# Optimization experiments

Measured on AMD Instinct MI355X. Metric: run time of the kernel, lower is better.

## Reference

```python
import jax, jax.numpy as jnp
import numpy as np

N = 12000       # num nodes
E = 384000      # num edges (avg degree 32)
F_IN = 512      # num_feats
H = 64          # gnn_hid_dim (== anchor_dim)
C = 7           # num_cls
SIGMA = 1.0


def setup_inputs() -> dict:
    key = jax.random.key(0)
    ks = jax.random.split(key, 9)
    scale = lambda fan_in: 1.0 / np.sqrt(fan_in)
    return {
        "x": jax.random.normal(ks[0], (N, F_IN), dtype=jnp.float32),
        "W1": jax.random.normal(ks[1], (F_IN, H), dtype=jnp.float32) * scale(F_IN),
        "b1": jnp.zeros((H,), dtype=jnp.float32),
        "W2": jax.random.normal(ks[2], (H, H), dtype=jnp.float32) * scale(H),
        "b2": jnp.zeros((H,), dtype=jnp.float32),
        "aux": jax.random.normal(ks[3], (H,), dtype=jnp.float32),
        "clf_W": jax.random.normal(ks[4], (2 * H, C), dtype=jnp.float32) * scale(2 * H),
        "clf_b": jnp.zeros((C,), dtype=jnp.float32),
        "edge_index": jax.random.randint(ks[5], (2, E), 0, N, dtype=jnp.int64),
    }


def gcn_conv(x, W, b, src, dst, n):
    # GCNConv: D^{-1/2} (A + I) D^{-1/2} X W + b, with self-loops
    h = x @ W                                                   # [N, out]
    deg = jax.ops.segment_sum(jnp.ones(src.shape[0], h.dtype), dst,
                              num_segments=n) + 1.0             # +1 for self-loop
    inv_sqrt = jax.lax.rsqrt(deg)
    norm = inv_sqrt[src] * inv_sqrt[dst]                        # [E]
    agg = jax.ops.segment_sum(h[src] * norm[:, None], dst, num_segments=n)
    agg = agg + h / deg[:, None]                                # self-loop term (norm = 1/deg)
    return agg + b


def reference(x, W1, b1, W2, b2, aux, clf_W, clf_b, edge_index):
    src, dst = edge_index[0], edge_index[1]
    n = x.shape[0]
    h = jax.nn.relu(gcn_conv(x, W1, b1, src, dst, n))
    h = gcn_conv(h, W2, b2, src, dst, n)                        # [N, H]
    # kernel aggregate: pairwise Gaussian kernel on cosine scores
    a = aux / jnp.maximum(jnp.linalg.norm(aux), 1e-12)          # F.normalize
    hn = jnp.maximum(jnp.linalg.norm(h, axis=-1), 1e-8)         # cosine_similarity eps
    score = (h @ a) / hn                                        # [N]
    diff = score[None, :] - score[:, None]                      # [N, N]
    kappa = jnp.exp(-(diff * diff) / (SIGMA * SIGMA))           # [N, N]
    z = (kappa @ h) / jnp.sum(kappa, axis=1, keepdims=True)     # [N, H]
    return jnp.concatenate([h, z], axis=-1) @ clf_W + clf_b     # [N, C]
```

## Files before the change

### kernel.cpp

```cpp
#include <hip/hip_runtime.h>
#include <hip/hip_bf16.h>

#define N_NODES 12000
#define N_EDGES 384000
#define F_IN 512
#define H 64
#define C_CLS 7
#define KTERMS 16
#define PAD 96
#define CSTR 32
#define MOM_BLKS 768
#define MSTR 1040
#define NB 4
#define GEMM_BLKS 188
#define FILL_BLKS 324

typedef __attribute__((ext_vector_type(8))) short bf16x8;
typedef __attribute__((ext_vector_type(4))) float f32x4;

__device__ __forceinline__ float wred_f(float x) {
    #pragma unroll
    for (int o = 32; o > 0; o >>= 1) x += __shfl_xor(x, o);
    return x;
}

__global__ __launch_bounds__(256) void init_k(const float* __restrict__ W1,
                                              unsigned short* __restrict__ w1Th,
                                              unsigned short* __restrict__ w1Tl,
                                              int* __restrict__ cur,
                                              double* __restrict__ M8) {
    int i = blockIdx.x * 256 + threadIdx.x;
    if (i < 64 * 512) {
        int n = i >> 9, k = i & 511;
        float v = W1[k * 64 + n];
        unsigned xb = __float_as_uint(v);
        float hf = __uint_as_float(xb & 0xffff0000u);
        w1Th[i] = (unsigned short)(xb >> 16);
        w1Tl[i] = (unsigned short)(__float_as_uint(v - hf) >> 16);
    }
    if (i < N_NODES) cur[i * CSTR] = 0;
    if (i < 8 * MSTR) M8[i] = 0.0;
}

__global__ __launch_bounds__(256) void k1_gemm_fill(const float* __restrict__ x,
                                                    const unsigned short* __restrict__ w1Th,
                                                    const unsigned short* __restrict__ w1Tl,
                                                    const int* __restrict__ ei,
                                                    float* __restrict__ hbuf,
                                                    int* __restrict__ cur,
                                                    int* __restrict__ csrc) {
    const int b = blockIdx.x, t = threadIdx.x;
    if (b < GEMM_BLKS) {
        __shared__ unsigned short wh[64 * 72];
        __shared__ unsigned short wl[64 * 72];
        const int l = t & 63, w = t >> 6;
        const int lm = l & 15, lk = l >> 4;
        const int i0 = b * 64;
        const int arow = min(i0 + w * 16 + lm, N_NODES - 1);
        const float* xrow = x + (size_t)arow * F_IN;
        f32x4 acc[4];
        #pragma unroll
        for (int c = 0; c < 4; ++c) acc[c] = (f32x4){0.f, 0.f, 0.f, 0.f};
        for (int kc = 0; kc < 8; ++kc) {
            #pragma unroll
            for (int q = 0; q < 2; ++q) {
                int idx = t + q * 256;
                int n = idx >> 3, kg = idx & 7;
                *(uint4*)(&wh[n * 72 + kg * 8]) =
                    *(const uint4*)(w1Th + n * 512 + kc * 64 + kg * 8);
                *(uint4*)(&wl[n * 72 + kg * 8]) =
                    *(const uint4*)(w1Tl + n * 512 + kc * 64 + kg * 8);
            }
            __syncthreads();
            #pragma unroll
            for (int ks = 0; ks < 2; ++ks) {
                float4 v0 = *(const float4*)(xrow + kc * 64 + ks * 32 + lk * 8);
                float4 v1 = *(const float4*)(xrow + kc * 64 + ks * 32 + lk * 8 + 4);
                float xv[8] = {v0.x, v0.y, v0.z, v0.w, v1.x, v1.y, v1.z, v1.w};
                bf16x8 ah, al;
                #pragma unroll
                for (int j = 0; j < 8; ++j) {
                    unsigned xb = __float_as_uint(xv[j]);
                    float hf = __uint_as_float(xb & 0xffff0000u);
                    ah[j] = (short)(xb >> 16);
                    al[j] = (short)(__float_as_uint(xv[j] - hf) >> 16);
                }
                #pragma unroll
                for (int c = 0; c < 4; ++c) {
                    bf16x8 bh = *(const bf16x8*)(&wh[(c * 16 + lm) * 72 + ks * 32 + lk * 8]);
                    bf16x8 bl = *(const bf16x8*)(&wl[(c * 16 + lm) * 72 + ks * 32 + lk * 8]);
                    acc[c] = __builtin_amdgcn_mfma_f32_16x16x32_bf16(ah, bh, acc[c], 0, 0, 0);
                    acc[c] = __builtin_amdgcn_mfma_f32_16x16x32_bf16(ah, bl, acc[c], 0, 0, 0);
                    acc[c] = __builtin_amdgcn_mfma_f32_16x16x32_bf16(al, bh, acc[c], 0, 0, 0);
                }
            }
            __syncthreads();
        }
        #pragma unroll
        for (int c = 0; c < 4; ++c) {
            #pragma unroll
            for (int r = 0; r < 4; ++r) {
                int row = i0 + w * 16 + lk * 4 + r;
                if (row < N_NODES)
                    hbuf[(size_t)row * H + c * 16 + lm] = acc[c][r];
            }
        }
    } else {
        for (int e = (b - GEMM_BLKS) * 256 + t; e < N_EDGES; e += FILL_BLKS * 256) {
            int s = ei[e];
            int d = ei[N_EDGES + e];
            int pos = atomicAdd(&cur[d * CSTR], 1);
            if (pos < PAD) csrc[d * PAD + pos] = s;
        }
    }
}

__global__ __launch_bounds__(256) void agg1_k(const float* __restrict__ hbuf,
                                              const float* __restrict__ b1,
                                              const int* __restrict__ cur,
                                              const int* __restrict__ csrc,
                                              float* __restrict__ h1) {
    __shared__ int2 sPair[NB * PAD];
    __shared__ int sDeg[NB];
    __shared__ float sIsd[NB];
    const int t = threadIdx.x, f = t & 63, w = t >> 6;
    const int base = blockIdx.x * NB;
    if (t < NB) {
        int d = cur[(base + t) * CSTR];
        sDeg[t] = min(d, PAD);
        sIsd[t] = rsqrtf((float)d + 1.f);
    }
    __syncthreads();
    for (int idx = t; idx < NB * PAD; idx += 256) {
        int n = idx / PAD, e = idx - n * PAD;
        if (e < sDeg[n]) {
            int s = csrc[(base + n) * PAD + e];
            sPair[idx] = make_int2(s, __float_as_int(rsqrtf((float)cur[s * CSTR] + 1.f)));
        }
    }
    __syncthreads();
    const int i = base + w;
    const int deg = sDeg[w];
    const float isd = sIsd[w];
    const int2* pp = sPair + w * PAD;
    float acc = 0.f;
    int e = 0;
    for (; e + 8 <= deg; e += 8) {
        int2 p0 = pp[e], p1 = pp[e+1], p2 = pp[e+2], p3 = pp[e+3];
        int2 p4 = pp[e+4], p5 = pp[e+5], p6 = pp[e+6], p7 = pp[e+7];
        acc += hbuf[p0.x * H + f] * __int_as_float(p0.y)
             + hbuf[p1.x * H + f] * __int_as_float(p1.y)
             + hbuf[p2.x * H + f] * __int_as_float(p2.y)
             + hbuf[p3.x * H + f] * __int_as_float(p3.y)
             + hbuf[p4.x * H + f] * __int_as_float(p4.y)
             + hbuf[p5.x * H + f] * __int_as_float(p5.y)
             + hbuf[p6.x * H + f] * __int_as_float(p6.y)
             + hbuf[p7.x * H + f] * __int_as_float(p7.y);
    }
    for (; e + 4 <= deg; e += 4) {
        int2 p0 = pp[e], p1 = pp[e+1], p2 = pp[e+2], p3 = pp[e+3];
        acc += hbuf[p0.x * H + f] * __int_as_float(p0.y)
             + hbuf[p1.x * H + f] * __int_as_float(p1.y)
             + hbuf[p2.x * H + f] * __int_as_float(p2.y)
             + hbuf[p3.x * H + f] * __int_as_float(p3.y);
    }
    for (; e < deg; ++e) {
        int2 p = pp[e];
        acc += hbuf[p.x * H + f] * __int_as_float(p.y);
    }
    float res = (acc + hbuf[i * H + f] * isd) * isd + b1[f];
    h1[i * H + f] = fmaxf(res, 0.f);
}

__global__ __launch_bounds__(256) void agg2_k(const float* __restrict__ h1,
                                              const float* __restrict__ W2,
                                              const float* __restrict__ b2,
                                              const float* __restrict__ aux,
                                              const int* __restrict__ cur,
                                              const int* __restrict__ csrc,
                                              float* __restrict__ h2,
                                              float* __restrict__ score) {
    __shared__ float w2s[64 * 64];
    __shared__ int2 sPair[NB * PAD];
    __shared__ int sDeg[NB];
    __shared__ float sIsd[NB];
    __shared__ float anorm[64];
    __shared__ float gsh[NB * 64];
    const int t = threadIdx.x, f = t & 63, w = t >> 6;
    const int base = blockIdx.x * NB;
    #pragma unroll
    for (int q = 0; q < 4; ++q) {
        int idx = t + q * 256;
        int r = idx >> 4, c4 = idx & 15;
        *(float4*)(&w2s[r * 64 + c4 * 4]) = *(const float4*)(W2 + r * H + c4 * 4);
    }
    if (t < NB) {
        int d = cur[(base + t) * CSTR];
        sDeg[t] = min(d, PAD);
        sIsd[t] = rsqrtf((float)d + 1.f);
    }
    if (t < 64) {
        float av = aux[t];
        anorm[t] = av * rsqrtf(fmaxf(wred_f(av * av), 1e-24f));
    }
    __syncthreads();
    for (int idx = t; idx < NB * PAD; idx += 256) {
        int n = idx / PAD, e = idx - n * PAD;
        if (e < sDeg[n]) {
            int s = csrc[(base + n) * PAD + e];
            sPair[idx] = make_int2(s, __float_as_int(rsqrtf((float)cur[s * CSTR] + 1.f)));
        }
    }
    __syncthreads();
    const int i = base + w;
    const int deg = sDeg[w];
    const float isd = sIsd[w];
    const int2* pp = sPair + w * PAD;
    float acc = 0.f;
    int e = 0;
    for (; e + 8 <= deg; e += 8) {
        int2 p0 = pp[e], p1 = pp[e+1], p2 = pp[e+2], p3 = pp[e+3];
        int2 p4 = pp[e+4], p5 = pp[e+5], p6 = pp[e+6], p7 = pp[e+7];
        acc += h1[p0.x * H + f] * __int_as_float(p0.y)
             + h1[p1.x * H + f] * __int_as_float(p1.y)
             + h1[p2.x * H + f] * __int_as_float(p2.y)
             + h1[p3.x * H + f] * __int_as_float(p3.y)
             + h1[p4.x * H + f] * __int_as_float(p4.y)
             + h1[p5.x * H + f] * __int_as_float(p5.y)
             + h1[p6.x * H + f] * __int_as_float(p6.y)
             + h1[p7.x * H + f] * __int_as_float(p7.y);
    }
    for (; e + 4 <= deg; e += 4) {
        int2 p0 = pp[e], p1 = pp[e+1], p2 = pp[e+2], p3 = pp[e+3];
        acc += h1[p0.x * H + f] * __int_as_float(p0.y)
             + h1[p1.x * H + f] * __int_as_float(p1.y)
             + h1[p2.x * H + f] * __int_as_float(p2.y)
             + h1[p3.x * H + f] * __int_as_float(p3.y);
    }
    for (; e < deg; ++e) {
        int2 p = pp[e];
        acc += h1[p.x * H + f] * __int_as_float(p.y);
    }
    float g = (acc + h1[i * H + f] * isd) * isd;
    gsh[w * 64 + f] = g;
    __builtin_amdgcn_wave_barrier();
    float hv = b2[f];
    #pragma unroll 16
    for (int k = 0; k < 64; ++k) hv += gsh[w * 64 + k] * w2s[k * 64 + f];
    h2[i * H + f] = hv;
    float dp = wred_f(hv * anorm[f]);
    float nn = wred_f(hv * hv);
    if (f == 0) score[i] = dp / fmaxf(sqrtf(nn), 1e-8f);
}

__global__ __launch_bounds__(256) void momden_k(const float* __restrict__ h2,
                                                const float* __restrict__ score,
                                                double* __restrict__ M8) {
    const int t = threadIdx.x, f = t & 63, g = t >> 6;
    float accM[KTERMS], accD[KTERMS];
    #pragma unroll
    for (int k = 0; k < KTERMS; ++k) { accM[k] = 0.f; accD[k] = 0.f; }
    for (int j = blockIdx.x * 4 + g; j < N_NODES; j += MOM_BLKS * 4) {
        float sj = score[j];
        float wj = expf(-sj * sj);
        float hv = h2[j * H + f];
        float tm = wj * hv, td = wj;
        #pragma unroll
        for (int k = 0; k < KTERMS; ++k) {
            accM[k] += tm; tm *= sj;
            accD[k] += td; td *= sj;
        }
    }
    __shared__ float Msh[4 * KTERMS * 64];
    __shared__ float Dsh[4 * KTERMS];
    #pragma unroll
    for (int k = 0; k < KTERMS; ++k) Msh[(g * KTERMS + k) * 64 + f] = accM[k];
    if (f == 0) {
        #pragma unroll
        for (int k = 0; k < KTERMS; ++k) Dsh[g * KTERMS + k] = accD[k];
    }
    __syncthreads();
    double* Mc = M8 + (size_t)(blockIdx.x & 7) * MSTR;
    for (int idx = t; idx < KTERMS * 64; idx += 256) {
        int k = idx >> 6, ff = idx & 63;
        float sum = Msh[(0 * KTERMS + k) * 64 + ff] + Msh[(1 * KTERMS + k) * 64 + ff]
                  + Msh[(2 * KTERMS + k) * 64 + ff] + Msh[(3 * KTERMS + k) * 64 + ff];
        unsafeAtomicAdd(&Mc[idx], (double)sum);
    }
    if (t < KTERMS) {
        float sum = Dsh[t] + Dsh[KTERMS + t] + Dsh[2 * KTERMS + t] + Dsh[3 * KTERMS + t];
        unsafeAtomicAdd(&Mc[1024 + t], (double)sum);
    }
}

__global__ __launch_bounds__(256) void final_k(const float* __restrict__ h2,
                                               const float* __restrict__ score,
                                               const double* __restrict__ M8,
                                               const float* __restrict__ clfW,
                                               const float* __restrict__ clfb,
                                               float* __restrict__ out) {
    __shared__ float Ms[KTERMS * 64];
    __shared__ float m0s[KTERMS];
    __shared__ float cw[128 * C_CLS];
    __shared__ float cb[8];
    __shared__ float zh[4 * 128];
    const int t = threadIdx.x, f = t & 63, w = t >> 6;
    for (int idx = t; idx < KTERMS * 64; idx += 256) {
        double s = 0.0;
        #pragma unroll
        for (int c = 0; c < 8; ++c) s += M8[(size_t)c * MSTR + idx];
        Ms[idx] = (float)s;
    }
    if (t < KTERMS) {
        double s = 0.0;
        #pragma unroll
        for (int c = 0; c < 8; ++c) s += M8[(size_t)c * MSTR + 1024 + t];
        m0s[t] = (float)s;
    }
    for (int idx = t; idx < 128 * C_CLS; idx += 256) cw[idx] = clfW[idx];
    if (t < C_CLS) cb[t] = clfb[t];
    __syncthreads();
    const int base = blockIdx.x * 16;
    for (int q = 0; q < 4; ++q) {
        int i = base + q * 4 + w;
        float s = score[i];
        float c = expf(-s * s);
        float t2 = 2.f * s;
        float num = 0.f, den = 0.f;
        #pragma unroll
        for (int k = 0; k < KTERMS; ++k) {
            num += c * Ms[k * 64 + f];
            den += c * m0s[k];
            c *= t2 * (1.0f / (float)(k + 1));
        }
        zh[w * 128 + f] = h2[i * H + f];
        zh[w * 128 + 64 + f] = num / den;
        __builtin_amdgcn_wave_barrier();
        if (f < C_CLS) {
            float o = cb[f];
            #pragma unroll 8
            for (int u = 0; u < 128; ++u) o += zh[w * 128 + u] * cw[u * C_CLS + f];
            out[(size_t)i * C_CLS + f] = o;
        }
        __builtin_amdgcn_wave_barrier();
    }
}

extern "C" void kernel_launch(void* const* d_in, const int* in_sizes, int n_in,
                              void* d_out, int out_size, void* d_ws, size_t ws_size,
                              hipStream_t stream) {
    (void)in_sizes; (void)n_in; (void)out_size; (void)ws_size;
    const float* x    = (const float*)d_in[0];
    const float* W1   = (const float*)d_in[1];
    const float* b1   = (const float*)d_in[2];
    const float* W2   = (const float*)d_in[3];
    const float* b2   = (const float*)d_in[4];
    const float* aux  = (const float*)d_in[5];
    const float* clfW = (const float*)d_in[6];
    const float* clfb = (const float*)d_in[7];
    const int*   ei   = (const int*)d_in[8];
    float* out = (float*)d_out;
    char* ws = (char*)d_ws;

    float*  hbuf  = (float*)(ws + 0);
    float*  h1    = (float*)(ws + 3072000);
    float*  h2    = (float*)(ws + 6144000);
    float*  score = (float*)(ws + 9216000);
    int*    csrc  = (int*)  (ws + 9264000);
    int*    cur   = (int*)  (ws + 13872000);
    double* M8    = (double*)(ws + 15408000);
    unsigned short* w1Th = (unsigned short*)(ws + 15474560);
    unsigned short* w1Tl = (unsigned short*)(ws + 15540096);

    init_k<<<128, 256, 0, stream>>>(W1, w1Th, w1Tl, cur, M8);
    k1_gemm_fill<<<GEMM_BLKS + FILL_BLKS, 256, 0, stream>>>(x, w1Th, w1Tl, ei,
                                                            hbuf, cur, csrc);
    agg1_k<<<N_NODES / NB, 256, 0, stream>>>(hbuf, b1, cur, csrc, h1);
    agg2_k<<<N_NODES / NB, 256, 0, stream>>>(h1, W2, b2, aux, cur, csrc, h2, score);
    momden_k<<<MOM_BLKS, 256, 0, stream>>>(h2, score, M8);
    final_k<<<750, 256, 0, stream>>>(h2, score, M8, clfW, clfb, out);
}
```

Measured before the change: 93.66 us.

## Fuse moment accumulation into second aggregation kernel and widen final blocks

The separate moment/denominator kernel is removed. Each agg2 block now computes the per-node power-series terms for its 4 nodes right after the score, reduces them in shared memory (aliased over the W2 tile) and adds them with fp64 atomics into 16 stripes instead of 8. This saves one kernel launch and a second pass over h2 and score. The cost is that atomic traffic grows from 768 blocks' worth of partial sums to 3000 blocks' worth, which may contend on L2. final_k now uses 250 blocks of 48 nodes each, to amortise the larger 16-stripe reduction it repeats in every block.

New measurement: 107.2 us. +14.4%, slower.

```diff
diff --git a/kernel.cpp b/kernel.cpp
--- a/kernel.cpp
+++ b/kernel.cpp
@@ -9,7 +9,7 @@
 #define KTERMS 16
 #define PAD 96
 #define CSTR 32
-#define MOM_BLKS 768
+#define NSTRIPE 16
 #define MSTR 1040
 #define NB 4
 #define GEMM_BLKS 188
@@ -28,7 +28,7 @@
                                               unsigned short* __restrict__ w1Th,
                                               unsigned short* __restrict__ w1Tl,
                                               int* __restrict__ cur,
-                                              double* __restrict__ M8) {
+                                              double* __restrict__ M16) {
     int i = blockIdx.x * 256 + threadIdx.x;
     if (i < 64 * 512) {
         int n = i >> 9, k = i & 511;
@@ -39,7 +39,7 @@
         w1Tl[i] = (unsigned short)(__float_as_uint(v - hf) >> 16);
     }
     if (i < N_NODES) cur[i * CSTR] = 0;
-    if (i < 8 * MSTR) M8[i] = 0.0;
+    for (int j = i; j < NSTRIPE * MSTR; j += 32768) M16[j] = 0.0;
 }
 
 __global__ __launch_bounds__(256) void k1_gemm_fill(const float* __restrict__ x,
@@ -172,20 +172,24 @@
     h1[i * H + f] = fmaxf(res, 0.f);
 }
 
-__global__ __launch_bounds__(256) void agg2_k(const float* __restrict__ h1,
-                                              const float* __restrict__ W2,
-                                              const float* __restrict__ b2,
-                                              const float* __restrict__ aux,
-                                              const int* __restrict__ cur,
-                                              const int* __restrict__ csrc,
-                                              float* __restrict__ h2,
-                                              float* __restrict__ score) {
-    __shared__ float w2s[64 * 64];
-    __shared__ int2 sPair[NB * PAD];
-    __shared__ int sDeg[NB];
-    __shared__ float sIsd[NB];
-    __shared__ float anorm[64];
-    __shared__ float gsh[NB * 64];
+__global__ __launch_bounds__(256) void agg2m_k(const float* __restrict__ h1,
+                                               const float* __restrict__ W2,
+                                               const float* __restrict__ b2,
+                                               const float* __restrict__ aux,
+                                               const int* __restrict__ cur,
+                                               const int* __restrict__ csrc,
+                                               float* __restrict__ h2,
+                                               float* __restrict__ score,
+                                               double* __restrict__ M16) {
+    __shared__ __align__(16) char smem[20768];
+    float* w2s   = (float*)smem;
+    int2*  sPair = (int2*)(smem + 16384);
+    int*   sDeg  = (int*)(smem + 19456);
+    float* sIsd  = (float*)(smem + 19472);
+    float* anorm = (float*)(smem + 19488);
+    float* gsh   = (float*)(smem + 19744);
+    float* Msh   = (float*)smem;
+    float* Dsh   = (float*)(smem + 16384);
     const int t = threadIdx.x, f = t & 63, w = t >> 6;
     const int base = blockIdx.x * NB;
     #pragma unroll
@@ -250,37 +254,20 @@
     h2[i * H + f] = hv;
     float dp = wred_f(hv * anorm[f]);
     float nn = wred_f(hv * hv);
-    if (f == 0) score[i] = dp / fmaxf(sqrtf(nn), 1e-8f);
-}
-
-__global__ __launch_bounds__(256) void momden_k(const float* __restrict__ h2,
-                                                const float* __restrict__ score,
-                                                double* __restrict__ M8) {
-    const int t = threadIdx.x, f = t & 63, g = t >> 6;
-    float accM[KTERMS], accD[KTERMS];
+    float sc = dp / fmaxf(sqrtf(nn), 1e-8f);
+    if (f == 0) score[i] = sc;
+    __syncthreads();
+    float wj = expf(-sc * sc);
+    float tm = wj * hv;
     #pragma unroll
-    for (int k = 0; k < KTERMS; ++k) { accM[k] = 0.f; accD[k] = 0.f; }
-    for (int j = blockIdx.x * 4 + g; j < N_NODES; j += MOM_BLKS * 4) {
-        float sj = score[j];
-        float wj = expf(-sj * sj);
-        float hv = h2[j * H + f];
-        float tm = wj * hv, td = wj;
-        #pragma unroll
-        for (int k = 0; k < KTERMS; ++k) {
-            accM[k] += tm; tm *= sj;
-            accD[k] += td; td *= sj;
-        }
-    }
-    __shared__ float Msh[4 * KTERMS * 64];
-    __shared__ float Dsh[4 * KTERMS];
-    #pragma unroll
-    for (int k = 0; k < KTERMS; ++k) Msh[(g * KTERMS + k) * 64 + f] = accM[k];
+    for (int k = 0; k < KTERMS; ++k) { Msh[(w * KTERMS + k) * 64 + f] = tm; tm *= sc; }
     if (f == 0) {
-        #pragma unroll
-        for (int k = 0; k < KTERMS; ++k) Dsh[g * KTERMS + k] = accD[k];
-    }
-    __syncthreads();
-    double* Mc = M8 + (size_t)(blockIdx.x & 7) * MSTR;
+        float td = wj;
+        #pragma unroll
+        for (int k = 0; k < KTERMS; ++k) { Dsh[w * KTERMS + k] = td; td *= sc; }
+    }
+    __syncthreads();
+    double* Mc = M16 + (size_t)(blockIdx.x & (NSTRIPE - 1)) * MSTR;
     for (int idx = t; idx < KTERMS * 64; idx += 256) {
         int k = idx >> 6, ff = idx & 63;
         float sum = Msh[(0 * KTERMS + k) * 64 + ff] + Msh[(1 * KTERMS + k) * 64 + ff]
@@ -295,7 +282,7 @@
 
 __global__ __launch_bounds__(256) void final_k(const float* __restrict__ h2,
                                                const float* __restrict__ score,
-                                               const double* __restrict__ M8,
+                                               const double* __restrict__ M16,
                                                const float* __restrict__ clfW,
                                                const float* __restrict__ clfb,
                                                float* __restrict__ out) {
@@ -308,20 +295,20 @@
     for (int idx = t; idx < KTERMS * 64; idx += 256) {
         double s = 0.0;
         #pragma unroll
-        for (int c = 0; c < 8; ++c) s += M8[(size_t)c * MSTR + idx];
+        for (int c = 0; c < NSTRIPE; ++c) s += M16[(size_t)c * MSTR + idx];
         Ms[idx] = (float)s;
     }
     if (t < KTERMS) {
         double s = 0.0;
         #pragma unroll
-        for (int c = 0; c < 8; ++c) s += M8[(size_t)c * MSTR + 1024 + t];
+        for (int c = 0; c < NSTRIPE; ++c) s += M16[(size_t)c * MSTR + 1024 + t];
         m0s[t] = (float)s;
     }
     for (int idx = t; idx < 128 * C_CLS; idx += 256) cw[idx] = clfW[idx];
     if (t < C_CLS) cb[t] = clfb[t];
     __syncthreads();
-    const int base = blockIdx.x * 16;
-    for (int q = 0; q < 4; ++q) {
+    const int base = blockIdx.x * 48;
+    for (int q = 0; q < 12; ++q) {
         int i = base + q * 4 + w;
         float s = score[i];
         float c = expf(-s * s);
@@ -368,15 +355,15 @@
     float*  score = (float*)(ws + 9216000);
     int*    csrc  = (int*)  (ws + 9264000);
     int*    cur   = (int*)  (ws + 13872000);
-    double* M8    = (double*)(ws + 15408000);
-    unsigned short* w1Th = (unsigned short*)(ws + 15474560);
-    unsigned short* w1Tl = (unsigned short*)(ws + 15540096);
-
-    init_k<<<128, 256, 0, stream>>>(W1, w1Th, w1Tl, cur, M8);
+    double* M16   = (double*)(ws + 15408000);
+    unsigned short* w1Th = (unsigned short*)(ws + 15541120);
+    unsigned short* w1Tl = (unsigned short*)(ws + 15606656);
+
+    init_k<<<128, 256, 0, stream>>>(W1, w1Th, w1Tl, cur, M16);
     k1_gemm_fill<<<GEMM_BLKS + FILL_BLKS, 256, 0, stream>>>(x, w1Th, w1Tl, ei,
                                                             hbuf, cur, csrc);
     agg1_k<<<N_NODES / NB, 256, 0, stream>>>(hbuf, b1, cur, csrc, h1);
-    agg2_k<<<N_NODES / NB, 256, 0, stream>>>(h1, W2, b2, aux, cur, csrc, h2, score);
-    momden_k<<<MOM_BLKS, 256, 0, stream>>>(h2, score, M8);
-    final_k<<<750, 256, 0, stream>>>(h2, score, M8, clfW, clfb, out);
-}
+    agg2m_k<<<N_NODES / NB, 256, 0, stream>>>(h1, W2, b2, aux, cur, csrc,
+                                              h2, score, M16);
+    final_k<<<250, 256, 0, stream>>>(h2, score, M16, clfW, clfb, out);
+}
```
